# Optimization experiments

Measured on AMD Instinct MI355X. Metric: run time of the kernel, lower is better.

The kernel has to match this reference:

```python
import jax, jax.numpy as jnp
import numpy as np

VX = 1.0 / 3.2
VY = 1.0 / 3.2
X_MIN, Y_MIN = -40.0, -20.0
NX, NY = 256, 256  # grid: (40-(-40))/VX, (60-(-20))/VY
X_OFF = VX / 2.0 + X_MIN
Y_OFF = VY / 2.0 + Y_MIN


def setup_inputs() -> dict:
    key = jax.random.key(0)
    ks = jax.random.split(key, 14)
    B = 8
    Ma, Pa, Ca = 60000, 20, 5
    Mr, Pr, Cr = 80000, 32, 3
    Da, Dr, Co = 64, 64, 32
    voxels_agent = jax.random.normal(ks[0], (Ma, Pa, Ca), jnp.float32)
    coors_agent = jnp.stack([
        jax.random.randint(ks[1], (Ma,), 0, B),
        jax.random.randint(ks[2], (Ma,), 0, NY),
        jax.random.randint(ks[3], (Ma,), 0, NX)], axis=-1).astype(jnp.int32)
    num_points_agent = jax.random.randint(ks[4], (Ma,), 1, Pa + 1).astype(jnp.int32)
    voxels_rg = jax.random.normal(ks[5], (Mr, Pr, Cr), jnp.float32)
    coors_rg = jnp.stack([
        jax.random.randint(ks[6], (Mr,), 0, B),
        jax.random.randint(ks[7], (Mr,), 0, NY),
        jax.random.randint(ks[8], (Mr,), 0, NX)], axis=-1).astype(jnp.int32)
    num_points_rg = jax.random.randint(ks[9], (Mr,), 1, Pr + 1).astype(jnp.int32)
    w_agent = 0.02 * jax.random.normal(ks[10], (Ca + 5, Da), jnp.float32)
    b_agent = jnp.zeros((Da,), jnp.float32)
    w_rg = 0.02 * jax.random.normal(ks[11], (Cr + 5, Dr), jnp.float32)
    b_rg = jnp.zeros((Dr,), jnp.float32)
    conv_w = 0.02 * jax.random.normal(ks[12], (3, 3, Da + Dr, Co), jnp.float32)
    conv_b = jnp.zeros((Co,), jnp.float32)
    return dict(voxels_agent=voxels_agent, coors_agent=coors_agent,
                num_points_agent=num_points_agent, voxels_rg=voxels_rg,
                coors_rg=coors_rg, num_points_rg=num_points_rg,
                w_agent=w_agent, b_agent=b_agent, w_rg=w_rg, b_rg=b_rg,
                conv_w=conv_w, conv_b=conv_b, batch_size=B)


def _pillar_vfe(voxels, coors, num_points, W, b):
    # voxels [M,P,C]; coors [M,3]=(batch,y,x); num_points [M]
    M, P, C = voxels.shape
    mask = (jnp.arange(P)[None, :] < num_points[:, None]).astype(voxels.dtype)[..., None]  # [M,P,1]
    npts = jnp.maximum(num_points, 1).astype(voxels.dtype)[:, None, None]
    xyz = voxels[..., :3]
    mean = jnp.sum(xyz * mask, axis=1, keepdims=True) / npts          # pillar cluster mean
    f_cluster = xyz - mean                                            # [M,P,3]
    cx = coors[:, 2].astype(voxels.dtype)[:, None]
    cy = coors[:, 1].astype(voxels.dtype)[:, None]
    f_cx = voxels[..., 0] - (cx * VX + X_OFF)                         # offset from pillar center
    f_cy = voxels[..., 1] - (cy * VY + Y_OFF)
    feats = jnp.concatenate([voxels, f_cluster,
                             jnp.stack([f_cx, f_cy], axis=-1)], axis=-1) * mask  # [M,P,C+5]
    h = jax.nn.relu(feats @ W + b)                                    # [M,P,D]
    return jnp.max(h * mask, axis=1)                                  # [M,D]


def _scatter(feats, coors, B):
    # scatter pillar features into dense BEV canvas [B,NY,NX,D]
    D = feats.shape[1]
    idx = coors[:, 0] * (NY * NX) + coors[:, 1] * NX + coors[:, 2]
    canvas = jnp.zeros((B * NY * NX, D), feats.dtype).at[idx].set(feats)
    return canvas.reshape(B, NY, NX, D)


def reference(voxels_agent, coors_agent, num_points_agent, voxels_rg, coors_rg,
              num_points_rg, w_agent, b_agent, w_rg, b_rg, conv_w, conv_b,
              batch_size):
    pa = _pillar_vfe(voxels_agent, coors_agent, num_points_agent, w_agent, b_agent)
    ca = _scatter(pa, coors_agent, batch_size)
    pr = _pillar_vfe(voxels_rg, coors_rg, num_points_rg, w_rg, b_rg)
    cr = _scatter(pr, coors_rg, batch_size)
    x = jnp.concatenate([ca, cr], axis=-1)                            # [B,NY,NX,128] NHWC
    y = jax.lax.conv_general_dilated(x, conv_w, (1, 1), 'SAME',
                                     dimension_numbers=('NHWC', 'HWIO', 'NHWC'))
    return y + conv_b                                                 # [B,NY,NX,32]
```

## Files before the change

kernel.cpp:

```cpp
#include <hip/hip_runtime.h>
#include <hip/hip_bf16.h>

#define MA 60000
#define PA 20
#define CA 5
#define MR 80000
#define PR 32
#define CR 3
#define NXg 256
#define NYg 256
#define NB 8
#define NCELL (NB * NYg * NXg)

typedef __bf16 bf16x8 __attribute__((ext_vector_type(8)));
typedef float  f32x4  __attribute__((ext_vector_type(4)));
typedef float  f4     __attribute__((ext_vector_type(4)));
typedef float  f2     __attribute__((ext_vector_type(2)));

__device__ __forceinline__ unsigned short f2bf(float f) {
    unsigned int u = __float_as_uint(f);
    u += 0x7fffu + ((u >> 16) & 1u);
    return (unsigned short)(u >> 16);
}

__global__ void __launch_bounds__(256) prep_kernel(int* __restrict__ win,
                                                   const float* __restrict__ conv_w,
                                                   unsigned short* __restrict__ bp) {
    int bid = blockIdx.x, tid = threadIdx.x;
    if (bid < 4096) {
        win[bid * 256 + tid] = -1;
    } else {
        int i = (bid - 4096) * 256 + tid;
        int j    = i & 7;
        int lane = (i >> 3) & 63;
        int nt   = (i >> 9) & 1;
        int kk   = (i >> 10) & 3;
        int tap  = i >> 12;
        int n = nt * 16 + (lane & 15);
        int k = kk * 32 + (lane >> 4) * 8 + j;
        bp[i] = f2bf(conv_w[(tap * 128 + k) * 32 + n]);
    }
}

template <int CIN, int CF, int PMAX, int PMAXp>
__device__ __forceinline__ void vfe_body(
    int bid, const float* __restrict__ vox, const int* __restrict__ coors,
    const int* __restrict__ npts, const float* __restrict__ W,
    const float* __restrict__ bias, unsigned short* __restrict__ feat,
    int* __restrict__ win, int M, int which, f4* sq)
{
    constexpr int PC   = PMAX * CIN;
    constexpr int NF4v = PC / 4;
    constexpr int SR   = PMAXp * CIN;
    constexpr int SR4  = SR / 4;
    constexpr int PP4  = PMAXp / 4;

    float* sf = (float*)sq;
    int tid  = threadIdx.x;
    int wv   = tid >> 6;
    int lane = tid & 63;
    int base = bid * 64;
    int cnt  = M - base; cnt = cnt > 64 ? 64 : cnt;

    {
        const f4* gv = (const f4*)vox + (size_t)base * NF4v;
        int totf4 = cnt * NF4v;
        for (int i = tid; i < totf4; i += 256) {
            f4 v = gv[i];
            int e = i * 4;
            int p = e / PC;
            int u = e - p * PC;
#pragma unroll
            for (int t = 0; t < 4; ++t) {
                int uu = u + t;
                int pt = uu / CIN;
                int c  = uu - pt * CIN;
                sf[p * SR + c * PMAXp + pt] = v[t];
            }
        }
    }

    float wc[CF];
#pragma unroll
    for (int c = 0; c < CF; ++c) wc[c] = W[c * 64 + lane];
    float bd = bias[lane];
    f2 we2[CIN];
    we2[0] = (f2){wc[0] + wc[CIN + 0] + wc[CIN + 3], wc[0] + wc[CIN + 0] + wc[CIN + 3]};
    we2[1] = (f2){wc[1] + wc[CIN + 1] + wc[CIN + 4], wc[1] + wc[CIN + 1] + wc[CIN + 4]};
    we2[2] = (f2){wc[2] + wc[CIN + 2], wc[2] + wc[CIN + 2]};
#pragma unroll
    for (int c = 3; c < CIN; ++c) we2[c] = (f2){wc[c], wc[c]};

    __syncthreads();

    if (tid < cnt) {
        int np = npts[base + tid];
        np = np < 1 ? 1 : (np > PMAX ? PMAX : np);
        int np8 = (np + 7) & ~7;
        float v0[CIN];
#pragma unroll
        for (int c = 0; c < CIN; ++c) v0[c] = sf[tid * SR + c * PMAXp];
        for (int p = np; p < np8; ++p)
#pragma unroll
            for (int c = 0; c < CIN; ++c)
                sf[tid * SR + c * PMAXp + p] = v0[c];
    }
    __syncthreads();

    int np_n = 1, cb_n = 0, cy_n = 0, cx_n = 0;
    if (wv < cnt) {
        np_n = npts[base + wv];
        cb_n = coors[(base + wv) * 3 + 0];
        cy_n = coors[(base + wv) * 3 + 1];
        cx_n = coors[(base + wv) * 3 + 2];
    }

    for (int pi = wv; pi < cnt; pi += 4) {
        int np = np_n, cb = cb_n, cy = cy_n, cx = cx_n;
        int pn = pi + 4;
        if (pn < cnt) {
            np_n = npts[base + pn];
            cb_n = coors[(base + pn) * 3 + 0];
            cy_n = coors[(base + pn) * 3 + 1];
            cx_n = coors[(base + pn) * 3 + 2];
        }
        np = np < 1 ? 1 : (np > PMAX ? PMAX : np);
        int nblk = (np + 7) >> 3;
        float kf = (float)(nblk * 8 - np);

        const f4* pf4 = sq + pi * SR4;
        const float* pf = sf + pi * SR;
        float x0 = pf[0], y0 = pf[PMAXp], z0 = pf[2 * PMAXp];

        f2 sx2 = {0.f, 0.f}, sy2 = {0.f, 0.f}, sz2 = {0.f, 0.f};
        f2 b2  = {-1e30f, -1e30f};

        for (int g = 0; g < nblk; ++g) {
            f4 lo[CIN], hi[CIN];
#pragma unroll
            for (int c = 0; c < CIN; ++c) {
                lo[c] = pf4[c * PP4 + g * 2];
                hi[c] = pf4[c * PP4 + g * 2 + 1];
            }
#pragma unroll
            for (int h = 0; h < 2; ++h) {
#pragma unroll
                for (int j = 0; j < 2; ++j) {
                    f2 x2 = h ? (f2){hi[0][2*j], hi[0][2*j+1]} : (f2){lo[0][2*j], lo[0][2*j+1]};
                    f2 y2 = h ? (f2){hi[1][2*j], hi[1][2*j+1]} : (f2){lo[1][2*j], lo[1][2*j+1]};
                    f2 z2 = h ? (f2){hi[2][2*j], hi[2][2*j+1]} : (f2){lo[2][2*j], lo[2][2*j+1]};
                    sx2 += x2; sy2 += y2; sz2 += z2;
                    f2 d2 = x2 * we2[0] + y2 * we2[1] + z2 * we2[2];
#pragma unroll
                    for (int c = 3; c < CIN; ++c) {
                        f2 e2 = h ? (f2){hi[c][2*j], hi[c][2*j+1]} : (f2){lo[c][2*j], lo[c][2*j+1]};
                        d2 += e2 * we2[c];
                    }
                    b2 = __builtin_elementwise_max(b2, d2);
                }
            }
        }

        float sx = sx2[0] + sx2[1] - kf * x0;
        float sy = sy2[0] + sy2[1] - kf * y0;
        float sz = sz2[0] + sz2[1] - kf * z0;
        float sbest = fmaxf(b2[0], b2[1]);

        float inv = 1.0f / (float)np;
        float mx = sx * inv, my = sy * inv, mz = sz * inv;
        float xo = (float)cx * 0.3125f + (-39.84375f);
        float yo = (float)cy * 0.3125f + (-19.84375f);
        float off = bd - (mx * wc[CIN + 0] + my * wc[CIN + 1] + mz * wc[CIN + 2])
                       - xo * wc[CIN + 3] - yo * wc[CIN + 4];
        float best = fmaxf(0.0f, sbest + off);

        feat[(size_t)(base + pi) * 64 + lane] = f2bf(best);

        if (lane == 0) {
            atomicMax(&win[((cb * NYg + cy) * NXg + cx) * 2 + which], base + pi);
        }
    }
}

__global__ void __launch_bounds__(256) vfe_all(
    const float* __restrict__ vox_a, const int* __restrict__ coor_a,
    const int* __restrict__ np_a, const float* __restrict__ w_a,
    const float* __restrict__ b_a, unsigned short* __restrict__ feat_a,
    const float* __restrict__ vox_r, const int* __restrict__ coor_r,
    const int* __restrict__ np_r, const float* __restrict__ w_r,
    const float* __restrict__ b_r, unsigned short* __restrict__ feat_r,
    int* __restrict__ win)
{
    __shared__ f4 sq[64 * 30];
    constexpr int NBA = (MA + 63) / 64;
    int bid = blockIdx.x;
    if (bid < NBA)
        vfe_body<CA, CA + 5, PA, 24>(bid, vox_a, coor_a, np_a, w_a, b_a,
                                     feat_a, win, MA, 0, sq);
    else
        vfe_body<CR, CR + 5, PR, 32>(bid - NBA, vox_r, coor_r, np_r, w_r, b_r,
                                     feat_r, win, MR, 1, sq);
}

__global__ void __launch_bounds__(256) conv_kernel(
    const unsigned short* __restrict__ feat_a,
    const unsigned short* __restrict__ feat_r,
    const int2* __restrict__ win2,
    const unsigned short* __restrict__ bpack,
    const float* __restrict__ conv_b,
    float* __restrict__ out)
{
    __shared__ uint4 sA[396 * 5];

    int tid  = threadIdx.x;
    int lane = tid & 63;
    int wv   = tid >> 6;
    int bid  = blockIdx.x;
    int xg = bid & 3, yg = (bid >> 2) & 63, b = bid >> 8;
    int x0 = xg * 64, y0 = yg * 4;
    int mrow = lane & 15, quad = lane >> 4;

    int wA[2] = {-1, -1}, wR[2] = {-1, -1};
#pragma unroll
    for (int r = 0; r < 2; ++r) {
        int cell = tid + r * 256;
        if (cell < 396) {
            int iy = cell / 66, ix = cell - iy * 66;
            int yy = y0 - 1 + iy, xx = x0 - 1 + ix;
            if ((unsigned)yy < 256u && (unsigned)xx < 256u) {
                int2 w2 = win2[(((b << 8) + yy) << 8) + xx];
                wA[r] = w2.x; wR[r] = w2.y;
            }
        }
    }

    f32x4 acc0[4], acc1[4];
#pragma unroll
    for (int mt = 0; mt < 4; ++mt) {
        acc0[mt] = (f32x4){0.f, 0.f, 0.f, 0.f};
        acc1[mt] = (f32x4){0.f, 0.f, 0.f, 0.f};
    }

#pragma unroll
    for (int ph = 0; ph < 4; ++ph) {
        const unsigned short* feat = (ph < 2) ? feat_a : feat_r;
        const int half = (ph & 1) * 32;

#pragma unroll
        for (int r = 0; r < 2; ++r) {
            int cell = tid + r * 256;
            if (cell < 396) {
                int w = (ph < 2) ? wA[r] : wR[r];
                uint4* dst = &sA[cell * 5];
                if (w >= 0) {
                    const uint4* src = (const uint4*)(feat + ((long)w << 6) + half);
                    dst[0] = src[0]; dst[1] = src[1];
                    dst[2] = src[2]; dst[3] = src[3];
                } else {
                    uint4 zz = {0, 0, 0, 0};
                    dst[0] = zz; dst[1] = zz; dst[2] = zz; dst[3] = zz;
                }
            }
        }
        __syncthreads();

#pragma unroll
        for (int tap = 0; tap < 9; ++tap) {
            const int dyo = tap / 3, dxo = tap % 3;
            const unsigned short* bp = bpack + tap * 4096 + ph * 1024 + lane * 8;
            bf16x8 bn0 = *(const bf16x8*)(bp);
            bf16x8 bn1 = *(const bf16x8*)(bp + 512);
            int iy = wv + dyo;
#pragma unroll
            for (int mt = 0; mt < 4; ++mt) {
                int ix = mt * 16 + mrow + dxo;
                bf16x8 a = *(const bf16x8*)(&sA[(iy * 66 + ix) * 5 + quad]);
                acc0[mt] = __builtin_amdgcn_mfma_f32_16x16x32_bf16(a, bn0, acc0[mt], 0, 0, 0);
                acc1[mt] = __builtin_amdgcn_mfma_f32_16x16x32_bf16(a, bn1, acc1[mt], 0, 0, 0);
            }
        }
        __syncthreads();
    }

    int col = lane & 15;
    float bias0 = conv_b[col];
    float bias1 = conv_b[col + 16];
    int cellbase = ((((b << 8) + y0 + wv)) << 8) + x0;
#pragma unroll
    for (int mt = 0; mt < 4; ++mt) {
#pragma unroll
        for (int r = 0; r < 4; ++r) {
            int cell = cellbase + mt * 16 + quad * 4 + r;
            float* o = out + (long)cell * 32;
            o[col]      = acc0[mt][r] + bias0;
            o[col + 16] = acc1[mt][r] + bias1;
        }
    }
}

extern "C" void kernel_launch(void* const* d_in, const int* in_sizes, int n_in,
                              void* d_out, int out_size, void* d_ws, size_t ws_size,
                              hipStream_t stream)
{
    const float* vox_a  = (const float*)d_in[0];
    const int*   coor_a = (const int*)d_in[1];
    const int*   np_a   = (const int*)d_in[2];
    const float* vox_r  = (const float*)d_in[3];
    const int*   coor_r = (const int*)d_in[4];
    const int*   np_r   = (const int*)d_in[5];
    const float* w_a    = (const float*)d_in[6];
    const float* b_a    = (const float*)d_in[7];
    const float* w_r    = (const float*)d_in[8];
    const float* b_r    = (const float*)d_in[9];
    const float* conv_w = (const float*)d_in[10];
    const float* conv_b = (const float*)d_in[11];
    float* out = (float*)d_out;

    char* ws = (char*)d_ws;
    unsigned short* feat_a = (unsigned short*)(ws);
    unsigned short* feat_r = (unsigned short*)(ws + 7680000);
    int* win               = (int*)(ws + 17920000);
    unsigned short* bpack  = (unsigned short*)(ws + 17920000 + 4194304);

    hipLaunchKernelGGL(prep_kernel, dim3(4096 + 144), dim3(256), 0, stream,
                       win, conv_w, bpack);
    hipLaunchKernelGGL(vfe_all, dim3((MA + 63) / 64 + (MR + 63) / 64), dim3(256), 0, stream,
                       vox_a, coor_a, np_a, w_a, b_a, feat_a,
                       vox_r, coor_r, np_r, w_r, b_r, feat_r, win);
    hipLaunchKernelGGL(conv_kernel, dim3(2048), dim3(256), 0, stream,
                       feat_a, feat_r, (const int2*)win, bpack, conv_b, out);
}
```

Measured before the change: 209.7 us.

## Register-prefetch next conv phase, shrink VFE blocks, move weight packing into VFE kernel

The conv kernel now loads the next phase's feature rows into registers before the current phase's MFMA loop, so the gather latency overlaps with compute instead of stalling before each LDS fill. The VFE kernel processes 32 pillars per block instead of 64, which doubles the block count and halves shared memory per block to improve occupancy and load balance. Conv weight packing moves from the init kernel into extra blocks of the VFE launch, and the win init uses 16-byte stores. The trade-offs are more registers in the conv kernel and less per-block reuse of weight loads in VFE.

```diff
diff --git a/kernel.cpp b/kernel.cpp
--- a/kernel.cpp
+++ b/kernel.cpp
@@ -23,14 +23,174 @@
     return (unsigned short)(u >> 16);
 }
 
-__global__ void __launch_bounds__(256) prep_kernel(int* __restrict__ win,
-                                                   const float* __restrict__ conv_w,
-                                                   unsigned short* __restrict__ bp) {
-    int bid = blockIdx.x, tid = threadIdx.x;
-    if (bid < 4096) {
-        win[bid * 256 + tid] = -1;
+__global__ void __launch_bounds__(256) prep_kernel(uint4* __restrict__ win4) {
+    uint4 m1 = {0xFFFFFFFFu, 0xFFFFFFFFu, 0xFFFFFFFFu, 0xFFFFFFFFu};
+    win4[blockIdx.x * 256 + threadIdx.x] = m1;
+}
+
+template <int CIN, int CF, int PMAX, int PMAXp>
+__device__ __forceinline__ void vfe_body(
+    int bid, const float* __restrict__ vox, const int* __restrict__ coors,
+    const int* __restrict__ npts, const float* __restrict__ W,
+    const float* __restrict__ bias, unsigned short* __restrict__ feat,
+    int* __restrict__ win, int M, int which, f4* sq)
+{
+    constexpr int G    = 32;
+    constexpr int PC   = PMAX * CIN;
+    constexpr int NF4v = PC / 4;
+    constexpr int SR   = PMAXp * CIN;
+    constexpr int SR4  = SR / 4;
+    constexpr int PP4  = PMAXp / 4;
+
+    float* sf = (float*)sq;
+    int tid  = threadIdx.x;
+    int wv   = tid >> 6;
+    int lane = tid & 63;
+    int base = bid * G;
+    int cnt  = M - base; cnt = cnt > G ? G : cnt;
+
+    {
+        const f4* gv = (const f4*)vox + (size_t)base * NF4v;
+        int totf4 = cnt * NF4v;
+        for (int i = tid; i < totf4; i += 256) {
+            f4 v = gv[i];
+            int e = i * 4;
+            int p = e / PC;
+            int u = e - p * PC;
+#pragma unroll
+            for (int t = 0; t < 4; ++t) {
+                int uu = u + t;
+                int pt = uu / CIN;
+                int c  = uu - pt * CIN;
+                sf[p * SR + c * PMAXp + pt] = v[t];
+            }
+        }
+    }
+
+    float wc[CF];
+#pragma unroll
+    for (int c = 0; c < CF; ++c) wc[c] = W[c * 64 + lane];
+    float bd = bias[lane];
+    f2 we2[CIN];
+    we2[0] = (f2){wc[0] + wc[CIN + 0] + wc[CIN + 3], wc[0] + wc[CIN + 0] + wc[CIN + 3]};
+    we2[1] = (f2){wc[1] + wc[CIN + 1] + wc[CIN + 4], wc[1] + wc[CIN + 1] + wc[CIN + 4]};
+    we2[2] = (f2){wc[2] + wc[CIN + 2], wc[2] + wc[CIN + 2]};
+#pragma unroll
+    for (int c = 3; c < CIN; ++c) we2[c] = (f2){wc[c], wc[c]};
+
+    __syncthreads();
+
+    if (tid < cnt) {
+        int np = npts[base + tid];
+        np = np < 1 ? 1 : (np > PMAX ? PMAX : np);
+        int np8 = (np + 7) & ~7;
+        float v0[CIN];
+#pragma unroll
+        for (int c = 0; c < CIN; ++c) v0[c] = sf[tid * SR + c * PMAXp];
+        for (int p = np; p < np8; ++p)
+#pragma unroll
+            for (int c = 0; c < CIN; ++c)
+                sf[tid * SR + c * PMAXp + p] = v0[c];
+    }
+    __syncthreads();
+
+    int np_n = 1, cb_n = 0, cy_n = 0, cx_n = 0;
+    if (wv < cnt) {
+        np_n = npts[base + wv];
+        cb_n = coors[(base + wv) * 3 + 0];
+        cy_n = coors[(base + wv) * 3 + 1];
+        cx_n = coors[(base + wv) * 3 + 2];
+    }
+
+    for (int pi = wv; pi < cnt; pi += 4) {
+        int np = np_n, cb = cb_n, cy = cy_n, cx = cx_n;
+        int pn = pi + 4;
+        if (pn < cnt) {
+            np_n = npts[base + pn];
+            cb_n = coors[(base + pn) * 3 + 0];
+            cy_n = coors[(base + pn) * 3 + 1];
+            cx_n = coors[(base + pn) * 3 + 2];
+        }
+        np = np < 1 ? 1 : (np > PMAX ? PMAX : np);
+        int nblk = (np + 7) >> 3;
+        float kf = (float)(nblk * 8 - np);
+
+        const f4* pf4 = sq + pi * SR4;
+        const float* pf = sf + pi * SR;
+        float x0 = pf[0], y0 = pf[PMAXp], z0 = pf[2 * PMAXp];
+
+        f2 sx2 = {0.f, 0.f}, sy2 = {0.f, 0.f}, sz2 = {0.f, 0.f};
+        f2 b2  = {-1e30f, -1e30f};
+
+        for (int g = 0; g < nblk; ++g) {
+            f4 lo[CIN], hi[CIN];
+#pragma unroll
+            for (int c = 0; c < CIN; ++c) {
+                lo[c] = pf4[c * PP4 + g * 2];
+                hi[c] = pf4[c * PP4 + g * 2 + 1];
+            }
+#pragma unroll
+            for (int h = 0; h < 2; ++h) {
+#pragma unroll
+                for (int j = 0; j < 2; ++j) {
+                    f2 x2 = h ? (f2){hi[0][2*j], hi[0][2*j+1]} : (f2){lo[0][2*j], lo[0][2*j+1]};
+                    f2 y2 = h ? (f2){hi[1][2*j], hi[1][2*j+1]} : (f2){lo[1][2*j], lo[1][2*j+1]};
+                    f2 z2 = h ? (f2){hi[2][2*j], hi[2][2*j+1]} : (f2){lo[2][2*j], lo[2][2*j+1]};
+                    sx2 += x2; sy2 += y2; sz2 += z2;
+                    f2 d2 = x2 * we2[0] + y2 * we2[1] + z2 * we2[2];
+#pragma unroll
+                    for (int c = 3; c < CIN; ++c) {
+                        f2 e2 = h ? (f2){hi[c][2*j], hi[c][2*j+1]} : (f2){lo[c][2*j], lo[c][2*j+1]};
+                        d2 += e2 * we2[c];
+                    }
+                    b2 = __builtin_elementwise_max(b2, d2);
+                }
+            }
+        }
+
+        float sx = sx2[0] + sx2[1] - kf * x0;
+        float sy = sy2[0] + sy2[1] - kf * y0;
+        float sz = sz2[0] + sz2[1] - kf * z0;
+        float sbest = fmaxf(b2[0], b2[1]);
+
+        float inv = 1.0f / (float)np;
+        float mx = sx * inv, my = sy * inv, mz = sz * inv;
+        float xo = (float)cx * 0.3125f + (-39.84375f);
+        float yo = (float)cy * 0.3125f + (-19.84375f);
+        float off = bd - (mx * wc[CIN + 0] + my * wc[CIN + 1] + mz * wc[CIN + 2])
+                       - xo * wc[CIN + 3] - yo * wc[CIN + 4];
+        float best = fmaxf(0.0f, sbest + off);
+
+        feat[(size_t)(base + pi) * 64 + lane] = f2bf(best);
+
+        if (lane == 0) {
+            atomicMax(&win[((cb * NYg + cy) * NXg + cx) * 2 + which], base + pi);
+        }
+    }
+}
+
+__global__ void __launch_bounds__(256) vfe_all(
+    const float* __restrict__ vox_a, const int* __restrict__ coor_a,
+    const int* __restrict__ np_a, const float* __restrict__ w_a,
+    const float* __restrict__ b_a, unsigned short* __restrict__ feat_a,
+    const float* __restrict__ vox_r, const int* __restrict__ coor_r,
+    const int* __restrict__ np_r, const float* __restrict__ w_r,
+    const float* __restrict__ b_r, unsigned short* __restrict__ feat_r,
+    int* __restrict__ win, const float* __restrict__ conv_w,
+    unsigned short* __restrict__ bp)
+{
+    __shared__ f4 sq[32 * 30];
+    constexpr int NBA = (MA + 31) / 32;
+    constexpr int NBR = (MR + 31) / 32;
+    int bid = blockIdx.x;
+    if (bid < NBA) {
+        vfe_body<CA, CA + 5, PA, 24>(bid, vox_a, coor_a, np_a, w_a, b_a,
+                                     feat_a, win, MA, 0, sq);
+    } else if (bid < NBA + NBR) {
+        vfe_body<CR, CR + 5, PR, 32>(bid - NBA, vox_r, coor_r, np_r, w_r, b_r,
+                                     feat_r, win, MR, 1, sq);
     } else {
-        int i = (bid - 4096) * 256 + tid;
+        int i = (bid - NBA - NBR) * 256 + threadIdx.x;
         int j    = i & 7;
         int lane = (i >> 3) & 63;
         int nt   = (i >> 9) & 1;
@@ -40,166 +200,6 @@
         int k = kk * 32 + (lane >> 4) * 8 + j;
         bp[i] = f2bf(conv_w[(tap * 128 + k) * 32 + n]);
     }
-}
-
-template <int CIN, int CF, int PMAX, int PMAXp>
-__device__ __forceinline__ void vfe_body(
-    int bid, const float* __restrict__ vox, const int* __restrict__ coors,
-    const int* __restrict__ npts, const float* __restrict__ W,
-    const float* __restrict__ bias, unsigned short* __restrict__ feat,
-    int* __restrict__ win, int M, int which, f4* sq)
-{
-    constexpr int PC   = PMAX * CIN;
-    constexpr int NF4v = PC / 4;
-    constexpr int SR   = PMAXp * CIN;
-    constexpr int SR4  = SR / 4;
-    constexpr int PP4  = PMAXp / 4;
-
-    float* sf = (float*)sq;
-    int tid  = threadIdx.x;
-    int wv   = tid >> 6;
-    int lane = tid & 63;
-    int base = bid * 64;
-    int cnt  = M - base; cnt = cnt > 64 ? 64 : cnt;
-
-    {
-        const f4* gv = (const f4*)vox + (size_t)base * NF4v;
-        int totf4 = cnt * NF4v;
-        for (int i = tid; i < totf4; i += 256) {
-            f4 v = gv[i];
-            int e = i * 4;
-            int p = e / PC;
-            int u = e - p * PC;
-#pragma unroll
-            for (int t = 0; t < 4; ++t) {
-                int uu = u + t;
-                int pt = uu / CIN;
-                int c  = uu - pt * CIN;
-                sf[p * SR + c * PMAXp + pt] = v[t];
-            }
-        }
-    }
-
-    float wc[CF];
-#pragma unroll
-    for (int c = 0; c < CF; ++c) wc[c] = W[c * 64 + lane];
-    float bd = bias[lane];
-    f2 we2[CIN];
-    we2[0] = (f2){wc[0] + wc[CIN + 0] + wc[CIN + 3], wc[0] + wc[CIN + 0] + wc[CIN + 3]};
-    we2[1] = (f2){wc[1] + wc[CIN + 1] + wc[CIN + 4], wc[1] + wc[CIN + 1] + wc[CIN + 4]};
-    we2[2] = (f2){wc[2] + wc[CIN + 2], wc[2] + wc[CIN + 2]};
-#pragma unroll
-    for (int c = 3; c < CIN; ++c) we2[c] = (f2){wc[c], wc[c]};
-
-    __syncthreads();
-
-    if (tid < cnt) {
-        int np = npts[base + tid];
-        np = np < 1 ? 1 : (np > PMAX ? PMAX : np);
-        int np8 = (np + 7) & ~7;
-        float v0[CIN];
-#pragma unroll
-        for (int c = 0; c < CIN; ++c) v0[c] = sf[tid * SR + c * PMAXp];
-        for (int p = np; p < np8; ++p)
-#pragma unroll
-            for (int c = 0; c < CIN; ++c)
-                sf[tid * SR + c * PMAXp + p] = v0[c];
-    }
-    __syncthreads();
-
-    int np_n = 1, cb_n = 0, cy_n = 0, cx_n = 0;
-    if (wv < cnt) {
-        np_n = npts[base + wv];
-        cb_n = coors[(base + wv) * 3 + 0];
-        cy_n = coors[(base + wv) * 3 + 1];
-        cx_n = coors[(base + wv) * 3 + 2];
-    }
-
-    for (int pi = wv; pi < cnt; pi += 4) {
-        int np = np_n, cb = cb_n, cy = cy_n, cx = cx_n;
-        int pn = pi + 4;
-        if (pn < cnt) {
-            np_n = npts[base + pn];
-            cb_n = coors[(base + pn) * 3 + 0];
-            cy_n = coors[(base + pn) * 3 + 1];
-            cx_n = coors[(base + pn) * 3 + 2];
-        }
-        np = np < 1 ? 1 : (np > PMAX ? PMAX : np);
-        int nblk = (np + 7) >> 3;
-        float kf = (float)(nblk * 8 - np);
-
-        const f4* pf4 = sq + pi * SR4;
-        const float* pf = sf + pi * SR;
-        float x0 = pf[0], y0 = pf[PMAXp], z0 = pf[2 * PMAXp];
-
-        f2 sx2 = {0.f, 0.f}, sy2 = {0.f, 0.f}, sz2 = {0.f, 0.f};
-        f2 b2  = {-1e30f, -1e30f};
-
-        for (int g = 0; g < nblk; ++g) {
-            f4 lo[CIN], hi[CIN];
-#pragma unroll
-            for (int c = 0; c < CIN; ++c) {
-                lo[c] = pf4[c * PP4 + g * 2];
-                hi[c] = pf4[c * PP4 + g * 2 + 1];
-            }
-#pragma unroll
-            for (int h = 0; h < 2; ++h) {
-#pragma unroll
-                for (int j = 0; j < 2; ++j) {
-                    f2 x2 = h ? (f2){hi[0][2*j], hi[0][2*j+1]} : (f2){lo[0][2*j], lo[0][2*j+1]};
-                    f2 y2 = h ? (f2){hi[1][2*j], hi[1][2*j+1]} : (f2){lo[1][2*j], lo[1][2*j+1]};
-                    f2 z2 = h ? (f2){hi[2][2*j], hi[2][2*j+1]} : (f2){lo[2][2*j], lo[2][2*j+1]};
-                    sx2 += x2; sy2 += y2; sz2 += z2;
-                    f2 d2 = x2 * we2[0] + y2 * we2[1] + z2 * we2[2];
-#pragma unroll
-                    for (int c = 3; c < CIN; ++c) {
-                        f2 e2 = h ? (f2){hi[c][2*j], hi[c][2*j+1]} : (f2){lo[c][2*j], lo[c][2*j+1]};
-                        d2 += e2 * we2[c];
-                    }
-                    b2 = __builtin_elementwise_max(b2, d2);
-                }
-            }
-        }
-
-        float sx = sx2[0] + sx2[1] - kf * x0;
-        float sy = sy2[0] + sy2[1] - kf * y0;
-        float sz = sz2[0] + sz2[1] - kf * z0;
-        float sbest = fmaxf(b2[0], b2[1]);
-
-        float inv = 1.0f / (float)np;
-        float mx = sx * inv, my = sy * inv, mz = sz * inv;
-        float xo = (float)cx * 0.3125f + (-39.84375f);
-        float yo = (float)cy * 0.3125f + (-19.84375f);
-        float off = bd - (mx * wc[CIN + 0] + my * wc[CIN + 1] + mz * wc[CIN + 2])
-                       - xo * wc[CIN + 3] - yo * wc[CIN + 4];
-        float best = fmaxf(0.0f, sbest + off);
-
-        feat[(size_t)(base + pi) * 64 + lane] = f2bf(best);
-
-        if (lane == 0) {
-            atomicMax(&win[((cb * NYg + cy) * NXg + cx) * 2 + which], base + pi);
-        }
-    }
-}
-
-__global__ void __launch_bounds__(256) vfe_all(
-    const float* __restrict__ vox_a, const int* __restrict__ coor_a,
-    const int* __restrict__ np_a, const float* __restrict__ w_a,
-    const float* __restrict__ b_a, unsigned short* __restrict__ feat_a,
-    const float* __restrict__ vox_r, const int* __restrict__ coor_r,
-    const int* __restrict__ np_r, const float* __restrict__ w_r,
-    const float* __restrict__ b_r, unsigned short* __restrict__ feat_r,
-    int* __restrict__ win)
-{
-    __shared__ f4 sq[64 * 30];
-    constexpr int NBA = (MA + 63) / 64;
-    int bid = blockIdx.x;
-    if (bid < NBA)
-        vfe_body<CA, CA + 5, PA, 24>(bid, vox_a, coor_a, np_a, w_a, b_a,
-                                     feat_a, win, MA, 0, sq);
-    else
-        vfe_body<CR, CR + 5, PR, 32>(bid - NBA, vox_r, coor_r, np_r, w_r, b_r,
-                                     feat_r, win, MR, 1, sq);
 }
 
 __global__ void __launch_bounds__(256) conv_kernel(
@@ -241,11 +241,19 @@
         acc1[mt] = (f32x4){0.f, 0.f, 0.f, 0.f};
     }
 
+    uint4 rbuf[2][4];
+#pragma unroll
+    for (int r = 0; r < 2; ++r) {
+        int cell = tid + r * 256;
+        if (cell < 396 && wA[r] >= 0) {
+            const uint4* src = (const uint4*)(feat_a + ((long)wA[r] << 6));
+#pragma unroll
+            for (int s = 0; s < 4; ++s) rbuf[r][s] = src[s];
+        }
+    }
+
 #pragma unroll
     for (int ph = 0; ph < 4; ++ph) {
-        const unsigned short* feat = (ph < 2) ? feat_a : feat_r;
-        const int half = (ph & 1) * 32;
-
 #pragma unroll
         for (int r = 0; r < 2; ++r) {
             int cell = tid + r * 256;
@@ -253,12 +261,25 @@
                 int w = (ph < 2) ? wA[r] : wR[r];
                 uint4* dst = &sA[cell * 5];
                 if (w >= 0) {
-                    const uint4* src = (const uint4*)(feat + ((long)w << 6) + half);
-                    dst[0] = src[0]; dst[1] = src[1];
-                    dst[2] = src[2]; dst[3] = src[3];
+                    dst[0] = rbuf[r][0]; dst[1] = rbuf[r][1];
+                    dst[2] = rbuf[r][2]; dst[3] = rbuf[r][3];
                 } else {
                     uint4 zz = {0, 0, 0, 0};
                     dst[0] = zz; dst[1] = zz; dst[2] = zz; dst[3] = zz;
+                }
+            }
+        }
+        if (ph < 3) {
+            const unsigned short* featn = (ph + 1 < 2) ? feat_a : feat_r;
+            const int halfn = ((ph + 1) & 1) * 32;
+#pragma unroll
+            for (int r = 0; r < 2; ++r) {
+                int cell = tid + r * 256;
+                int w = (ph + 1 < 2) ? wA[r] : wR[r];
+                if (cell < 396 && w >= 0) {
+                    const uint4* src = (const uint4*)(featn + ((long)w << 6) + halfn);
+#pragma unroll
+                    for (int s = 0; s < 4; ++s) rbuf[r][s] = src[s];
                 }
             }
         }
@@ -322,11 +343,11 @@
     int* win               = (int*)(ws + 17920000);
     unsigned short* bpack  = (unsigned short*)(ws + 17920000 + 4194304);
 
-    hipLaunchKernelGGL(prep_kernel, dim3(4096 + 144), dim3(256), 0, stream,
-                       win, conv_w, bpack);
-    hipLaunchKernelGGL(vfe_all, dim3((MA + 63) / 64 + (MR + 63) / 64), dim3(256), 0, stream,
+    hipLaunchKernelGGL(prep_kernel, dim3(1024), dim3(256), 0, stream, (uint4*)win);
+    constexpr int NBA = (MA + 31) / 32, NBR = (MR + 31) / 32;
+    hipLaunchKernelGGL(vfe_all, dim3(NBA + NBR + 144), dim3(256), 0, stream,
                        vox_a, coor_a, np_a, w_a, b_a, feat_a,
-                       vox_r, coor_r, np_r, w_r, b_r, feat_r, win);
+                       vox_r, coor_r, np_r, w_r, b_r, feat_r, win, conv_w, bpack);
     hipLaunchKernelGGL(conv_kernel, dim3(2048), dim3(256), 0, stream,
                        feat_a, feat_r, (const int2*)win, bpack, conv_b, out);
 }
```

New measurement: 248.8 us. 18.6% more time.
